# Performance work log

Measured on AMD Instinct MI355X. Metric: run time of the kernel, lower is better.

Reference implementation:

```python
import jax, jax.numpy as jnp
import numpy as np

TOPK_RATE = 0.1

def setup_inputs() -> dict:
    key = jax.random.key(0)
    k1, k2 = jax.random.split(key)
    B, C, H, W = 32, 256, 128, 128
    x = jax.random.normal(k1, (B, C, H, W), dtype=jnp.float32)
    w = jax.random.normal(k2, (1, C, 1, 1), dtype=jnp.float32) * 0.05
    b = jnp.zeros((1,), dtype=jnp.float32)
    return {"x": x, "w": w, "b": b}

def reference(x, w, b):
    B, C, H, W = x.shape
    # 1x1 conv to a single output channel == channel contraction
    scores = jnp.einsum('bchw,c->bhw', x, w[0, :, 0, 0]) + b[0]  # [B,H,W]
    flat = scores.reshape(B, H * W)
    topk = max(int(H * W * TOPK_RATE), 1)
    vals, _ = jax.lax.top_k(jnp.abs(flat), topk)  # [B, topk]
    return jnp.mean(vals, axis=1).reshape(-1, 1)  # [B,1]
```

## Files before the change

### kernel.cpp

```cpp
#include <hip/hip_runtime.h>
#include <hip/hip_bf16.h>
#include <stdint.h>

#define B_    32
#define C_    256
#define HW_   16384
#define K_TOP 1638

typedef float f32x2 __attribute__((ext_vector_type(2)));
typedef float f32x4 __attribute__((ext_vector_type(4)));

__global__ __launch_bounds__(256) void score_kernel(const float* __restrict__ x,
                                                    const float* __restrict__ w,
                                                    const float* __restrict__ bias,
                                                    float* __restrict__ scores) {
    const uint32_t tid  = blockIdx.x * 256u + threadIdx.x;
    const uint32_t bi   = tid >> 12;
    const uint32_t p4   = (tid & 4095u) << 2;
    const uint32_t toff = bi * (uint32_t)(C_ * HW_) + p4;

    const float* xc = x;
    f32x2 a0 = {0.f, 0.f};
    f32x2 a1 = {0.f, 0.f};

    #pragma unroll 8
    for (int c = 0; c < C_; ++c) {
        const f32x4 v  = __builtin_nontemporal_load(
                             reinterpret_cast<const f32x4*>(xc + toff));
        const float wc = w[c];
        const f32x2 wp = {wc, wc};
        f32x2 lo = __builtin_shufflevector(v, v, 0, 1);
        f32x2 hi = __builtin_shufflevector(v, v, 2, 3);
        asm("v_pk_fma_f32 %0, %1, %2, %0" : "+v"(a0) : "v"(lo), "s"(wp));
        asm("v_pk_fma_f32 %0, %1, %2, %0" : "+v"(a1) : "v"(hi), "s"(wp));
        xc += HW_;
    }

    const float bb = bias[0];
    f32x4 o;
    o[0] = fabsf(a0[0] + bb);
    o[1] = fabsf(a0[1] + bb);
    o[2] = fabsf(a1[0] + bb);
    o[3] = fabsf(a1[1] + bb);
    *reinterpret_cast<f32x4*>(scores + (bi * (uint32_t)HW_ + p4)) = o;
}

template <int NB>
__device__ __forceinline__ void find_crossing(const uint32_t* hist, int k,
                                              int* sh_bin, int* sh_k, int tid) {
    constexpr int G = NB >> 6;
    if (tid < 64) {
        const int lane = tid;
        uint32_t gs = 0;
        #pragma unroll
        for (int i = 0; i < G; ++i) {
            const int j = (i + lane) & (G - 1);
            gs += hist[lane * G + j];
        }
        uint32_t s = gs;
        #pragma unroll
        for (int off = 1; off < 64; off <<= 1) {
            uint32_t t = __shfl_down(s, off);
            s += (lane + off < 64) ? t : 0u;
        }
        uint32_t snext = __shfl_down(s, 1);
        if (lane == 63) snext = 0u;
        const bool mine = (s >= (uint32_t)k) && (snext < (uint32_t)k);
        const unsigned long long bal = __ballot(mine);
        const int g = __ffsll(bal) - 1;
        const uint32_t above_g = __shfl(snext, g);

        uint32_t hv = (lane < G) ? hist[g * G + lane] : 0u;
        uint32_t s2 = hv;
        #pragma unroll
        for (int off = 1; off < G; off <<= 1) {
            uint32_t t = __shfl_down(s2, off);
            s2 += (lane + off < G) ? t : 0u;
        }
        uint32_t s2next = __shfl_down(s2, 1);
        if (lane >= G - 1) s2next = 0u;
        const bool mine2 = (lane < G) &&
                           (above_g + s2 >= (uint32_t)k) &&
                           (above_g + s2next < (uint32_t)k);
        if (mine2) {
            *sh_bin = g * G + lane;
            *sh_k   = k - (int)(above_g + s2next);
        }
    }
    __syncthreads();
}

__global__ __launch_bounds__(1024) void topk_mean_kernel(const float* __restrict__ scores,
                                                         float* __restrict__ out) {
    const int tid = threadIdx.x;
    const int b   = blockIdx.x;

    __shared__ uint32_t hist[2048];
    __shared__ float    sumc[512];
    __shared__ float    red[16];
    __shared__ int      sh_bin, sh_k;

    const uint4* sv = reinterpret_cast<const uint4*>(scores) + (size_t)b * (HW_ / 4);
    uint32_t r[16];
    {
        uint4 q;
        q = sv[tid];        r[0]  = q.x; r[1]  = q.y; r[2]  = q.z; r[3]  = q.w;
        q = sv[tid + 1024]; r[4]  = q.x; r[5]  = q.y; r[6]  = q.z; r[7]  = q.w;
        q = sv[tid + 2048]; r[8]  = q.x; r[9]  = q.y; r[10] = q.z; r[11] = q.w;
        q = sv[tid + 3072]; r[12] = q.x; r[13] = q.y; r[14] = q.z; r[15] = q.w;
    }

    hist[tid] = 0u; hist[tid + 1024] = 0u;
    __syncthreads();

    #pragma unroll
    for (int i = 0; i < 16; ++i) atomicAdd(&hist[r[i] >> 20], 1u);
    __syncthreads();
    find_crossing<2048>(hist, K_TOP, &sh_bin, &sh_k, tid);
    const uint32_t B1 = (uint32_t)sh_bin;
    const int      k1 = sh_k;
    __syncthreads();

    hist[tid] = 0u; hist[tid + 1024] = 0u;
    __syncthreads();

    float sAbove = 0.f;
    #pragma unroll
    for (int i = 0; i < 16; ++i) {
        const uint32_t u  = r[i];
        const uint32_t b1 = u >> 20;
        if (b1 > B1)       sAbove += __uint_as_float(u);
        else if (b1 == B1) atomicAdd(&hist[(u >> 9) & 2047u], 1u);
    }
    __syncthreads();
    find_crossing<2048>(hist, k1, &sh_bin, &sh_k, tid);
    const uint32_t B2 = (uint32_t)sh_bin;
    const int      k2 = sh_k;
    __syncthreads();

    if (tid < 512) { hist[tid] = 0u; sumc[tid] = 0.f; }
    __syncthreads();

    #pragma unroll
    for (int i = 0; i < 16; ++i) {
        const uint32_t u = r[i];
        if ((u >> 20) == B1) {
            const uint32_t b2 = (u >> 9) & 2047u;
            if (b2 > B2) sAbove += __uint_as_float(u);
            else if (b2 == B2) {
                const uint32_t b3 = u & 511u;
                atomicAdd(&hist[b3], 1u);
                atomicAdd(&sumc[b3], __uint_as_float(u));
            }
        }
    }
    __syncthreads();
    find_crossing<512>(hist, k2, &sh_bin, &sh_k, tid);
    const uint32_t B3 = (uint32_t)sh_bin;
    const int      k3 = sh_k;
    __syncthreads();

    if (tid < 512 && tid > (int)B3) sAbove += sumc[tid];

    #pragma unroll
    for (int off = 32; off > 0; off >>= 1) sAbove += __shfl_down(sAbove, off);
    if ((tid & 63) == 0) red[tid >> 6] = sAbove;
    __syncthreads();

    if (tid == 0) {
        float tot = 0.f;
        #pragma unroll
        for (int i = 0; i < 16; ++i) tot += red[i];
        const float T = __uint_as_float((B1 << 20) | (B2 << 9) | B3);
        out[b] = (tot + (float)k3 * T) / (float)K_TOP;
    }
}

extern "C" void kernel_launch(void* const* d_in, const int* in_sizes, int n_in,
                              void* d_out, int out_size, void* d_ws, size_t ws_size,
                              hipStream_t stream) {
    const float* x    = (const float*)d_in[0];
    const float* w    = (const float*)d_in[1];
    const float* bias = (const float*)d_in[2];
    float*       out  = (float*)d_out;
    float*       scores = (float*)d_ws;

    score_kernel<<<512, 256, 0, stream>>>(x, w, bias, scores);
    topk_mean_kernel<<<B_, 1024, 0, stream>>>(scores, out);
}
```

Baseline: 95.78 us.

## Fuse score and top-k kernels via last-block-per-batch completion counter

Merges the channel-contraction kernel and the per-batch radix top-k kernel into one launch. Each block atomically increments a per-batch counter after writing its scores, and the last of the 16 blocks for that batch runs the three-pass histogram selection with 256 threads, holding 64 values per thread. This removes the second kernel launch and lets selection for early batches overlap with score computation for later ones. In exchange it adds a memset launch, and the selection runs with a quarter of the threads and much higher register pressure, which may lower occupancy in the bandwidth-bound score phase.

```diff
diff --git a/kernel.cpp b/kernel.cpp
--- a/kernel.cpp
+++ b/kernel.cpp
@@ -6,44 +6,10 @@
 #define C_    256
 #define HW_   16384
 #define K_TOP 1638
+#define BPB   16
 
 typedef float f32x2 __attribute__((ext_vector_type(2)));
 typedef float f32x4 __attribute__((ext_vector_type(4)));
-
-__global__ __launch_bounds__(256) void score_kernel(const float* __restrict__ x,
-                                                    const float* __restrict__ w,
-                                                    const float* __restrict__ bias,
-                                                    float* __restrict__ scores) {
-    const uint32_t tid  = blockIdx.x * 256u + threadIdx.x;
-    const uint32_t bi   = tid >> 12;
-    const uint32_t p4   = (tid & 4095u) << 2;
-    const uint32_t toff = bi * (uint32_t)(C_ * HW_) + p4;
-
-    const float* xc = x;
-    f32x2 a0 = {0.f, 0.f};
-    f32x2 a1 = {0.f, 0.f};
-
-    #pragma unroll 8
-    for (int c = 0; c < C_; ++c) {
-        const f32x4 v  = __builtin_nontemporal_load(
-                             reinterpret_cast<const f32x4*>(xc + toff));
-        const float wc = w[c];
-        const f32x2 wp = {wc, wc};
-        f32x2 lo = __builtin_shufflevector(v, v, 0, 1);
-        f32x2 hi = __builtin_shufflevector(v, v, 2, 3);
-        asm("v_pk_fma_f32 %0, %1, %2, %0" : "+v"(a0) : "v"(lo), "s"(wp));
-        asm("v_pk_fma_f32 %0, %1, %2, %0" : "+v"(a1) : "v"(hi), "s"(wp));
-        xc += HW_;
-    }
-
-    const float bb = bias[0];
-    f32x4 o;
-    o[0] = fabsf(a0[0] + bb);
-    o[1] = fabsf(a0[1] + bb);
-    o[2] = fabsf(a1[0] + bb);
-    o[3] = fabsf(a1[1] + bb);
-    *reinterpret_cast<f32x4*>(scores + (bi * (uint32_t)HW_ + p4)) = o;
-}
 
 template <int NB>
 __device__ __forceinline__ void find_crossing(const uint32_t* hist, int k,
@@ -90,59 +56,106 @@
     __syncthreads();
 }
 
-__global__ __launch_bounds__(1024) void topk_mean_kernel(const float* __restrict__ scores,
-                                                         float* __restrict__ out) {
-    const int tid = threadIdx.x;
-    const int b   = blockIdx.x;
-
+__global__ __launch_bounds__(256) void fused_kernel(const float* __restrict__ x,
+                                                    const float* __restrict__ w,
+                                                    const float* __restrict__ bias,
+                                                    float* __restrict__ scores,
+                                                    uint32_t* __restrict__ cnt,
+                                                    float* __restrict__ out) {
+    const uint32_t tid  = blockIdx.x * 256u + threadIdx.x;
+    const uint32_t bi   = tid >> 12;
+    const uint32_t p4   = (tid & 4095u) << 2;
+    const uint32_t toff = bi * (uint32_t)(C_ * HW_) + p4;
+
+    {
+        const float* xc = x;
+        f32x2 a0 = {0.f, 0.f};
+        f32x2 a1 = {0.f, 0.f};
+
+        #pragma unroll 8
+        for (int c = 0; c < C_; ++c) {
+            const f32x4 v  = __builtin_nontemporal_load(
+                                 reinterpret_cast<const f32x4*>(xc + toff));
+            const float wc = w[c];
+            const f32x2 wp = {wc, wc};
+            f32x2 lo = __builtin_shufflevector(v, v, 0, 1);
+            f32x2 hi = __builtin_shufflevector(v, v, 2, 3);
+            asm("v_pk_fma_f32 %0, %1, %2, %0" : "+v"(a0) : "v"(lo), "s"(wp));
+            asm("v_pk_fma_f32 %0, %1, %2, %0" : "+v"(a1) : "v"(hi), "s"(wp));
+            xc += HW_;
+        }
+
+        const float bb = bias[0];
+        f32x4 o;
+        o[0] = fabsf(a0[0] + bb);
+        o[1] = fabsf(a0[1] + bb);
+        o[2] = fabsf(a1[0] + bb);
+        o[3] = fabsf(a1[1] + bb);
+        *reinterpret_cast<f32x4*>(scores + (bi * (uint32_t)HW_ + p4)) = o;
+    }
+
+    __shared__ int      sh_last;
     __shared__ uint32_t hist[2048];
     __shared__ float    sumc[512];
-    __shared__ float    red[16];
+    __shared__ float    red[4];
     __shared__ int      sh_bin, sh_k;
 
-    const uint4* sv = reinterpret_cast<const uint4*>(scores) + (size_t)b * (HW_ / 4);
-    uint32_t r[16];
-    {
-        uint4 q;
-        q = sv[tid];        r[0]  = q.x; r[1]  = q.y; r[2]  = q.z; r[3]  = q.w;
-        q = sv[tid + 1024]; r[4]  = q.x; r[5]  = q.y; r[6]  = q.z; r[7]  = q.w;
-        q = sv[tid + 2048]; r[8]  = q.x; r[9]  = q.y; r[10] = q.z; r[11] = q.w;
-        q = sv[tid + 3072]; r[12] = q.x; r[13] = q.y; r[14] = q.z; r[15] = q.w;
-    }
-
-    hist[tid] = 0u; hist[tid + 1024] = 0u;
-    __syncthreads();
-
-    #pragma unroll
-    for (int i = 0; i < 16; ++i) atomicAdd(&hist[r[i] >> 20], 1u);
-    __syncthreads();
-    find_crossing<2048>(hist, K_TOP, &sh_bin, &sh_k, tid);
+    __syncthreads();
+    if (threadIdx.x == 0) {
+        __threadfence();
+        const uint32_t old = atomicAdd(&cnt[bi], 1u);
+        sh_last = (old == (uint32_t)(BPB - 1));
+    }
+    __syncthreads();
+    if (!sh_last) return;
+
+    __threadfence();
+
+    const int t = threadIdx.x;
+    const uint4* sv = reinterpret_cast<const uint4*>(scores) + (size_t)bi * (HW_ / 4);
+    uint32_t r[64];
+    #pragma unroll
+    for (int j = 0; j < 16; ++j) {
+        const uint4 q = sv[t + 256 * j];
+        r[4*j+0] = q.x; r[4*j+1] = q.y; r[4*j+2] = q.z; r[4*j+3] = q.w;
+    }
+
+    #pragma unroll
+    for (int i = t; i < 2048; i += 256) hist[i] = 0u;
+    __syncthreads();
+
+    #pragma unroll
+    for (int i = 0; i < 64; ++i) atomicAdd(&hist[r[i] >> 20], 1u);
+    __syncthreads();
+    find_crossing<2048>(hist, K_TOP, &sh_bin, &sh_k, t);
     const uint32_t B1 = (uint32_t)sh_bin;
     const int      k1 = sh_k;
     __syncthreads();
 
-    hist[tid] = 0u; hist[tid + 1024] = 0u;
+    #pragma unroll
+    for (int i = t; i < 2048; i += 256) hist[i] = 0u;
     __syncthreads();
 
     float sAbove = 0.f;
     #pragma unroll
-    for (int i = 0; i < 16; ++i) {
+    for (int i = 0; i < 64; ++i) {
         const uint32_t u  = r[i];
         const uint32_t b1 = u >> 20;
         if (b1 > B1)       sAbove += __uint_as_float(u);
         else if (b1 == B1) atomicAdd(&hist[(u >> 9) & 2047u], 1u);
     }
     __syncthreads();
-    find_crossing<2048>(hist, k1, &sh_bin, &sh_k, tid);
+    find_crossing<2048>(hist, k1, &sh_bin, &sh_k, t);
     const uint32_t B2 = (uint32_t)sh_bin;
     const int      k2 = sh_k;
     __syncthreads();
 
-    if (tid < 512) { hist[tid] = 0u; sumc[tid] = 0.f; }
-    __syncthreads();
-
-    #pragma unroll
-    for (int i = 0; i < 16; ++i) {
+    #pragma unroll
+    for (int i = t; i < 512; i += 256) { hist[i] = 0u; sumc[i] = 0.f; }
+    __syncthreads();
+
+    #pragma unroll
+    for (int i = 0; i < 64; ++i) {
         const uint32_t u = r[i];
         if ((u >> 20) == B1) {
             const uint32_t b2 = (u >> 9) & 2047u;
@@ -155,24 +168,23 @@
         }
     }
     __syncthreads();
-    find_crossing<512>(hist, k2, &sh_bin, &sh_k, tid);
+    find_crossing<512>(hist, k2, &sh_bin, &sh_k, t);
     const uint32_t B3 = (uint32_t)sh_bin;
     const int      k3 = sh_k;
     __syncthreads();
 
-    if (tid < 512 && tid > (int)B3) sAbove += sumc[tid];
+    #pragma unroll
+    for (int i = t; i < 512; i += 256) if (i > (int)B3) sAbove += sumc[i];
 
     #pragma unroll
     for (int off = 32; off > 0; off >>= 1) sAbove += __shfl_down(sAbove, off);
-    if ((tid & 63) == 0) red[tid >> 6] = sAbove;
-    __syncthreads();
-
-    if (tid == 0) {
-        float tot = 0.f;
-        #pragma unroll
-        for (int i = 0; i < 16; ++i) tot += red[i];
+    if ((t & 63) == 0) red[t >> 6] = sAbove;
+    __syncthreads();
+
+    if (t == 0) {
+        float tot = red[0] + red[1] + red[2] + red[3];
         const float T = __uint_as_float((B1 << 20) | (B2 << 9) | B3);
-        out[b] = (tot + (float)k3 * T) / (float)K_TOP;
+        out[bi] = (tot + (float)k3 * T) / (float)K_TOP;
     }
 }
 
@@ -183,8 +195,11 @@
     const float* w    = (const float*)d_in[1];
     const float* bias = (const float*)d_in[2];
     float*       out  = (float*)d_out;
-    float*       scores = (float*)d_ws;
-
-    score_kernel<<<512, 256, 0, stream>>>(x, w, bias, scores);
-    topk_mean_kernel<<<B_, 1024, 0, stream>>>(scores, out);
+
+    float*    scores = (float*)d_ws;
+    uint32_t* cnt    = (uint32_t*)((char*)d_ws +
+                                   (size_t)B_ * HW_ * sizeof(float));
+
+    hipMemsetAsync(cnt, 0, B_ * sizeof(uint32_t), stream);
+    fused_kernel<<<512, 256, 0, stream>>>(x, w, bias, scores, cnt, out);
 }
```

After: 137.9 us. +43.9%, slower.
